# Kernel optimization log

Measured on AMD Instinct MI355X. Metric: run time of the kernel, lower is better.

The kernel has to match this reference:

```python
import jax, jax.numpy as jnp
import numpy as np

N_WAY = 5
K_SHOT = 5
TEMPERATURE = 2.0
EPS = 1e-8


def _l2norm(x, axis):
    n = jnp.sqrt(jnp.sum(x * x, axis=axis, keepdims=True))
    return x / jnp.maximum(n, EPS)


def setup_inputs() -> dict:
    key = jax.random.key(0)
    k1, k2, k3, k4 = jax.random.split(key, 4)
    b, q, c, h, w = 4, 75, 640, 14, 14
    s = N_WAY * K_SHOT
    return {
        "support_xf": jax.random.normal(k1, (b, s, c, h, w), dtype=jnp.float32),
        "support_y": jax.random.randint(k2, (b, s), 0, N_WAY),
        "query_xf": jax.random.normal(k3, (b, q, c, h, w), dtype=jnp.float32),
        "query_y": jax.random.randint(k4, (b, q), 0, N_WAY),
    }


def _mn4_loss(support_xf, query_xf, query_y):
    b, q, c, h, w = query_xf.shape
    M = h * w  # M_q == M_s (k_shot averaging)
    # k-shot average: (b, N, k, c, h*w) -> (b, N, c, M)
    sup = support_xf.reshape(b, N_WAY, K_SHOT, c, M).mean(axis=2)
    qf = query_xf.reshape(b, q, c, M)
    # cosine similarity: normalize along channel dim
    sup_n = _l2norm(sup, axis=2)   # (b, N, c, M)
    qf_n = _l2norm(qf, axis=2)     # (b, q, c, M)
    # S: (b, q, N, M_q, M_s)
    S = jnp.einsum('bqcm,bncs->bqnms', qf_n, sup_n)

    NM = N_WAY * M
    # merged: (b, q, M_q, N*M_s)
    merged = jnp.transpose(S, (0, 1, 3, 2, 4)).reshape(b, q, M, NM)
    query_nearest = jnp.argmax(merged, axis=-1)               # (b, q, M_q)
    class_wise_max = S.max(axis=-1).max(axis=2) + 1.0          # (b, q, M_q)
    class_m = jax.nn.one_hot(query_nearest, NM, dtype=S.dtype) * class_wise_max[..., None]  # (b,q,M_q,NM)
    class_m_max = class_m.max(axis=-2)                         # (b, q, NM)
    support_nearest = jnp.argmax(class_m, axis=-2)             # (b, q, NM)
    support_nearest = jnp.where(class_m_max == 0, M + 1, support_nearest)
    # gather: back-pointer for each query position's chosen support index
    gathered = jnp.take_along_axis(support_nearest, query_nearest, axis=-1)  # (b, q, M_q)
    mask = (gathered == jnp.arange(M)[None, None, :])          # mutual-NN mask (b, q, M_q)
    query_mask = mask.astype(S.dtype) * TEMPERATURE

    # predict: masked sum of per-class best similarities over query positions
    predict = (S.max(axis=-1) * query_mask[:, :, None, :]).sum(axis=-1)  # (b, q, N)
    predict = predict.reshape(b * q, N_WAY)
    y = query_y.reshape(b * q)
    logp = jax.nn.log_softmax(predict, axis=-1)
    loss = -jnp.take_along_axis(logp, y[:, None], axis=1).mean()
    return loss


def reference(support_xf, support_y, query_xf, query_y):
    return _mn4_loss(support_xf, query_xf, query_y)
```

## Files before the change

kernel.cpp:

```cpp
#include <hip/hip_runtime.h>
#include <math.h>

#define NWAY 5
#define KSHOT 5
#define BB 4
#define QQ 75
#define CC 640
#define MM 196
#define BQ (BB*QQ)
#define MP 208
#define NCOL 1024
#define NREAL 980

#define BPK_OFF   0
#define BPK_SZF   (BB*NCOL*CC/2)
#define APK_OFF   (BPK_OFF + BPK_SZF)
#define APK_SZF   ((BQ*MP + 64)*CC/2)
#define GSTAT_OFF (APK_OFF + APK_SZF)
#define GSTAT_N   (BQ*NWAY*MP)
#define NRMS_OFF  (GSTAT_OFF + 2*GSTAT_N)
#define NRMS_SZ   (BB*NWAY*MM)
#define NRMQ_OFF  (NRMS_OFF + NRMS_SZ)
#define NRMQ_SZ   (BQ*MM)

typedef __attribute__((ext_vector_type(8))) _Float16 half8;
typedef __attribute__((ext_vector_type(4))) float floatx4;

__global__ void k_prep(const float* __restrict__ sx, const float* __restrict__ qx,
                       _Float16* __restrict__ Apk, _Float16* __restrict__ Bpk,
                       float* __restrict__ nrmq, float* __restrict__ nrms) {
    __shared__ float T[64 * 197];
    int t = threadIdx.x;
    int blk = blockIdx.x;
    if (blk < 3000) {
        int bq = blk / 10, cc = blk % 10;
        int c0 = cc * 64;
        const float* Q = qx + (size_t)bq * CC * MM + (size_t)c0 * MM;
        for (int idx = t; idx < 64 * MM; idx += 256) {
            int ci = idx / MM, m = idx - ci * MM;
            T[ci * 197 + m] = Q[idx];
        }
        __syncthreads();
        _Float16* out = Apk + (size_t)bq * MP * CC;
        int mloc = t >> 3, cj8 = t & 7;
        #pragma unroll
        for (int r = 0; r < 7; r++) {
            int mm = r * 32 + mloc;
            if (mm < MP) {
                half8 v;
                #pragma unroll
                for (int k = 0; k < 8; k++) {
                    float f = (mm < MM) ? T[(cj8 * 8 + k) * 197 + mm] : 0.f;
                    v[k] = (_Float16)f;
                }
                *(half8*)&out[(size_t)mm * CC + c0 + cj8 * 8] = v;
            }
        }
        if (t < MM) {
            float ss = 0.f;
            for (int ci = 0; ci < 64; ci++) { float v = T[ci * 197 + t]; ss += v * v; }
            atomicAdd(&nrmq[bq * MM + t], ss);
        }
    } else {
        int bb = blk - 3000;
        int bn = bb / 10, cc = bb % 10;
        int b = bn / NWAY, n = bn % NWAY;
        int c0 = cc * 64;
        const float* S = sx + (size_t)bn * KSHOT * CC * MM + (size_t)c0 * MM;
        for (int idx = t; idx < 64 * MM; idx += 256) {
            int ci = idx / MM, m = idx - ci * MM;
            float s = 0.f;
            #pragma unroll
            for (int k = 0; k < KSHOT; k++) s += S[(size_t)k * CC * MM + idx];
            T[ci * 197 + m] = s * 0.2f;
        }
        __syncthreads();
        _Float16* out = Bpk + ((size_t)b * NCOL + (size_t)n * MM) * CC;
        int mloc = t >> 3, cj8 = t & 7;
        #pragma unroll
        for (int r = 0; r < 7; r++) {
            int mm = r * 32 + mloc;
            if (mm < MM) {
                half8 v;
                #pragma unroll
                for (int k = 0; k < 8; k++)
                    v[k] = (_Float16)T[(cj8 * 8 + k) * 197 + mm];
                *(half8*)&out[(size_t)mm * CC + c0 + cj8 * 8] = v;
            }
        }
        if (t < MM) {
            float ss = 0.f;
            for (int ci = 0; ci < 64; ci++) { float v = T[ci * 197 + t]; ss += v * v; }
            atomicAdd(&nrms[bn * MM + t], ss);
        }
    }
}

__global__ __launch_bounds__(256, 3) void k_sim(
    const _Float16* __restrict__ Apk, const _Float16* __restrict__ Bpk,
    const float* __restrict__ nrms, unsigned long long* __restrict__ gstat)
{
    __shared__ __align__(16) _Float16 Lds[16384];
    int id = blockIdx.x;
    int x = id & 7, s = id >> 3;
    int sub = s & 15, bqg = s >> 4;
    int bq = x + (bqg << 3);
    if (bq >= BQ) return;
    int mblk = sub >> 3, cblk = sub & 7;
    int b = bq / QQ;

    int t = threadIdx.x, lane = t & 63, w = t >> 6;
    int q = lane >> 4, l15 = lane & 15;

    const _Float16* Ab = Apk + (size_t)bq * MP * CC + (size_t)(mblk * 128) * CC;
    const _Float16* Bb = Bpk + ((size_t)b * NCOL + (size_t)(cblk * 128)) * CC;
    const _Float16* base = (w < 2) ? Ab : Bb;

    int voff[8];
    #pragma unroll
    for (int p = 0; p < 8; p++) {
        int chunk = (w * 8 + p) * 64 + lane;
        if (chunk < 1024) {
            int m = chunk >> 3, j = chunk & 7;
            voff[p] = m * CC + ((j ^ (m & 7)) << 3);
        } else {
            int cb = chunk - 1024;
            int jl = cb >> 3, j = cb & 7;
            voff[p] = jl * CC + ((j ^ (jl & 7)) << 3);
        }
    }

    int arow[2], asw[2], brow[8], bsw[8];
    #pragma unroll
    for (int i = 0; i < 2; i++) {
        int m = w * 32 + i * 16 + l15;
        arow[i] = m * 64; asw[i] = m & 7;
    }
    #pragma unroll
    for (int jt = 0; jt < 8; jt++) {
        int jl = jt * 16 + l15;
        brow[jt] = 8192 + jl * 64; bsw[jt] = jl & 7;
    }

    floatx4 acc[2][8];
    #pragma unroll
    for (int i = 0; i < 2; i++)
        #pragma unroll
        for (int j = 0; j < 8; j++) acc[i][j] = (floatx4){0.f, 0.f, 0.f, 0.f};

    for (int c0 = 0; c0 < CC; c0 += 64) {
        #pragma unroll
        for (int p = 0; p < 8; p++)
            __builtin_amdgcn_global_load_lds(
                (const __attribute__((address_space(1))) void*)(base + voff[p] + c0),
                (__attribute__((address_space(3))) void*)(Lds + (w * 8 + p) * 512),
                16, 0, 0);
        __syncthreads();
        #pragma unroll
        for (int ks = 0; ks < 2; ks++) {
            int cj = ks * 4 + q;
            half8 af[2], bf[8];
            #pragma unroll
            for (int i = 0; i < 2; i++)
                af[i] = *(const half8*)&Lds[arow[i] + ((cj ^ asw[i]) << 3)];
            #pragma unroll
            for (int jt = 0; jt < 8; jt++)
                bf[jt] = *(const half8*)&Lds[brow[jt] + ((cj ^ bsw[jt]) << 3)];
            #pragma unroll
            for (int i = 0; i < 2; i++)
                #pragma unroll
                for (int jt = 0; jt < 8; jt++)
                    acc[i][jt] = __builtin_amdgcn_mfma_f32_16x16x32_f16(af[i], bf[jt], acc[i][jt], 0, 0, 0);
        }
        __syncthreads();
    }

    int wbase = cblk * 128;
    int clsLo = wbase / 196;
    float invv[8]; int ms8[8], isLo[8], valid[8];
    #pragma unroll
    for (int jt = 0; jt < 8; jt++) {
        int c = wbase + jt * 16 + l15;
        int cls = c / 196;
        ms8[jt] = c - cls * 196;
        isLo[jt] = (cls == clsLo);
        valid[jt] = (c < NREAL);
        invv[jt] = valid[jt] ? (1.0f / fmaxf(sqrtf(nrms[b * NREAL + c]), 1e-8f)) : 0.f;
    }
    #pragma unroll
    for (int i = 0; i < 2; i++) {
        #pragma unroll
        for (int r = 0; r < 4; r++) {
            unsigned long long keyLo = 0ULL, keyHi = 0ULL;
            #pragma unroll
            for (int jt = 0; jt < 8; jt++) {
                float v = acc[i][jt][r] * invv[jt];
                unsigned int ub = __float_as_uint(v);
                unsigned int su = (ub & 0x80000000u) ? ~ub : (ub | 0x80000000u);
                unsigned long long key = valid[jt]
                    ? (((unsigned long long)su << 32) |
                       (unsigned long long)(0xFFFFFFFFu - (unsigned int)ms8[jt]))
                    : 0ULL;
                if (isLo[jt]) keyLo = (key > keyLo) ? key : keyLo;
                else          keyHi = (key > keyHi) ? key : keyHi;
            }
            #pragma unroll
            for (int sft = 1; sft < 16; sft <<= 1) {
                unsigned long long oL = __shfl_xor(keyLo, sft, 64);
                unsigned long long oH = __shfl_xor(keyHi, sft, 64);
                if (oL > keyLo) keyLo = oL;
                if (oH > keyHi) keyHi = oH;
            }
            if (l15 == 0) {
                int gm = mblk * 128 + w * 32 + i * 16 + q * 4 + r;
                if (gm < MM) {
                    if (keyLo)
                        atomicMax(&gstat[((size_t)bq * NWAY + clsLo) * MP + gm], keyLo);
                    int clsHi = clsLo + 1;
                    if (keyHi && clsHi < NWAY)
                        atomicMax(&gstat[((size_t)bq * NWAY + clsHi) * MP + gm], keyHi);
                }
            }
        }
    }
}

__global__ void k_post(const unsigned long long* __restrict__ gstat,
                       const float* __restrict__ nrmq,
                       float* __restrict__ out, const int* __restrict__ qy) {
    int bq = blockIdx.x;
    int t = threadIdx.x;
    __shared__ float invq_s[MM];
    __shared__ float cm[NWAY * MM];
    __shared__ int   ca[NWAY * MM];
    __shared__ float gmax[MM];
    __shared__ int   jst[MM];
    __shared__ int   msk[MM];
    __shared__ float pred[NWAY];

    if (t < MM) invq_s[t] = 1.0f / fmaxf(sqrtf(nrmq[bq * MM + t]), 1e-8f);
    __syncthreads();

    for (int i = t; i < NWAY * MM; i += 256) {
        int n = i / MM, m = i - n * MM;
        unsigned long long key = gstat[((size_t)bq * NWAY + n) * MP + m];
        unsigned int hi = (unsigned int)(key >> 32);
        unsigned int bits = (hi & 0x80000000u) ? (hi ^ 0x80000000u) : ~hi;
        cm[i] = __uint_as_float(bits) * invq_s[m];
        ca[i] = (int)(0xFFFFFFFFu - (unsigned int)(key & 0xFFFFFFFFu));
    }
    __syncthreads();

    if (t < MM) {
        float bv = cm[t];
        int bj = ca[t];
        for (int n = 1; n < NWAY; n++) {
            float v = cm[n * MM + t];
            if (v > bv) { bv = v; bj = n * MM + ca[n * MM + t]; }
        }
        gmax[t] = bv; jst[t] = bj;
    }
    __syncthreads();

    if (t < MM) {
        int myj = jst[t];
        float myv = gmax[t];
        int lose = 0;
        for (int m2 = 0; m2 < MM; m2++) {
            if (jst[m2] == myj &&
                (gmax[m2] > myv || (gmax[m2] == myv && m2 < t))) lose = 1;
        }
        msk[t] = !lose;
    }
    __syncthreads();

    if (t < NWAY) {
        float p = 0.f;
        for (int m = 0; m < MM; m++) if (msk[m]) p += cm[t * MM + m];
        pred[t] = 2.0f * p;
    }
    __syncthreads();

    if (t == 0) {
        float pm = pred[0];
        for (int n = 1; n < NWAY; n++) pm = fmaxf(pm, pred[n]);
        float s = 0.f;
        for (int n = 0; n < NWAY; n++) s += expf(pred[n] - pm);
        float lse = pm + logf(s);
        int y = qy[bq];
        atomicAdd(out, (lse - pred[y]) * (1.0f / (BB * QQ)));
    }
}

extern "C" void kernel_launch(void* const* d_in, const int* in_sizes, int n_in,
                              void* d_out, int out_size, void* d_ws, size_t ws_size,
                              hipStream_t stream) {
    const float* sx = (const float*)d_in[0];
    const float* qx = (const float*)d_in[2];
    const int*   qy = (const int*)d_in[3];
    float* out = (float*)d_out;
    float* ws  = (float*)d_ws;

    _Float16* Bpk = (_Float16*)(ws + BPK_OFF);
    _Float16* Apk = (_Float16*)(ws + APK_OFF);
    unsigned long long* gstat = (unsigned long long*)(ws + GSTAT_OFF);
    float* nrms = ws + NRMS_OFF;
    float* nrmq = ws + NRMQ_OFF;

    hipMemsetAsync(gstat, 0, (size_t)(2 * GSTAT_N + NRMS_SZ + NRMQ_SZ) * 4, stream);
    hipMemsetAsync(out, 0, 4, stream);
    hipLaunchKernelGGL(k_prep, dim3(3200), dim3(256), 0, stream, sx, qx, Apk, Bpk, nrmq, nrms);
    hipLaunchKernelGGL(k_sim,  dim3(8 * 38 * 16), dim3(256), 0, stream, Apk, Bpk, nrms, gstat);
    hipLaunchKernelGGL(k_post, dim3(300), dim3(256), 0, stream, gstat, nrmq, out, qy);
}
```

Baseline: 447.0 us.

## Retile k_sim GEMM to 256x256 blocks with double-buffered LDS loads

Restructures the similarity GEMM so that each 512-thread block computes all 256 (padded) query rows against 256 support columns, replacing the earlier 128x128 tiles. The new tiling cuts redundant A/B reloads from global memory. LDS is double-buffered so the next 64-channel slice is prefetched while MFMAs run on the current one. The change also remaps block order per XCD, skips MFMA tiles for padded query rows, raises wave priority around the MFMAs, and only reduces the second-class key when a wave's column range crosses a class boundary. In exchange, LDS use rises to 128KB per block and each thread holds a larger accumulator set, which limits occupancy and may cause spills.

Result: slower. 1.070 ms (+139.4%).

```diff
diff --git a/kernel.cpp b/kernel.cpp
--- a/kernel.cpp
+++ b/kernel.cpp
@@ -96,128 +96,144 @@
     }
 }
 
-__global__ __launch_bounds__(256, 3) void k_sim(
+__global__ __launch_bounds__(512, 2) void k_sim(
     const _Float16* __restrict__ Apk, const _Float16* __restrict__ Bpk,
     const float* __restrict__ nrms, unsigned long long* __restrict__ gstat)
 {
-    __shared__ __align__(16) _Float16 Lds[16384];
-    int id = blockIdx.x;
-    int x = id & 7, s = id >> 3;
-    int sub = s & 15, bqg = s >> 4;
-    int bq = x + (bqg << 3);
-    if (bq >= BQ) return;
-    int mblk = sub >> 3, cblk = sub & 7;
+    __shared__ __align__(16) _Float16 Lds[65536];
+
+    int hw = blockIdx.x;
+    int logical = (hw & 7) * 150 + (hw >> 3);
+    int bq = logical >> 2, cblk = logical & 3;
     int b = bq / QQ;
 
-    int t = threadIdx.x, lane = t & 63, w = t >> 6;
-    int q = lane >> 4, l15 = lane & 15;
-
-    const _Float16* Ab = Apk + (size_t)bq * MP * CC + (size_t)(mblk * 128) * CC;
-    const _Float16* Bb = Bpk + ((size_t)b * NCOL + (size_t)(cblk * 128)) * CC;
-    const _Float16* base = (w < 2) ? Ab : Bb;
-
-    int voff[8];
+    int t = threadIdx.x, w = t >> 6, lane = t & 63;
+    int wm = w >> 2, wn = w & 3;
+    int q = lane >> 4, l15 = lane & 15, s7 = l15 & 7;
+
+    const _Float16* Ab = Apk + (size_t)bq * MP * CC;
+    const _Float16* Bb = Bpk + ((size_t)b * NCOL + (size_t)cblk * 256) * CC;
+
+    int voff[4];
+    {
+        int rr = t >> 3, slot = t & 7;
+        #pragma unroll
+        for (int a = 0; a < 4; a++) {
+            int r = a * 64 + rr;
+            voff[a] = r * CC + ((slot ^ (r & 7)) << 3);
+        }
+    }
+
+    int aoff[8], boff[4];
     #pragma unroll
-    for (int p = 0; p < 8; p++) {
-        int chunk = (w * 8 + p) * 64 + lane;
-        if (chunk < 1024) {
-            int m = chunk >> 3, j = chunk & 7;
-            voff[p] = m * CC + ((j ^ (m & 7)) << 3);
-        } else {
-            int cb = chunk - 1024;
-            int jl = cb >> 3, j = cb & 7;
-            voff[p] = jl * CC + ((j ^ (jl & 7)) << 3);
-        }
-    }
-
-    int arow[2], asw[2], brow[8], bsw[8];
+    for (int m = 0; m < 8; m++) aoff[m] = (wm * 128 + m * 16 + l15) * 64;
     #pragma unroll
-    for (int i = 0; i < 2; i++) {
-        int m = w * 32 + i * 16 + l15;
-        arow[i] = m * 64; asw[i] = m & 7;
-    }
+    for (int n = 0; n < 4; n++) boff[n] = 16384 + (wn * 64 + n * 16 + l15) * 64;
+
+    floatx4 acc[8][4];
     #pragma unroll
-    for (int jt = 0; jt < 8; jt++) {
-        int jl = jt * 16 + l15;
-        brow[jt] = 8192 + jl * 64; bsw[jt] = jl & 7;
-    }
-
-    floatx4 acc[2][8];
+    for (int m = 0; m < 8; m++)
+        #pragma unroll
+        for (int n = 0; n < 4; n++) acc[m][n] = (floatx4){0.f, 0.f, 0.f, 0.f};
+
+    #define STAGE(TT)                                                                  \
+        do {                                                                           \
+            int nb_ = ((TT) & 1) << 15;                                                \
+            int c0_ = (TT) * 64;                                                       \
+            _Pragma("unroll")                                                          \
+            for (int a = 0; a < 4; a++) {                                              \
+                __builtin_amdgcn_global_load_lds(                                      \
+                    (const __attribute__((address_space(1))) void*)(Ab + voff[a] + c0_),\
+                    (__attribute__((address_space(3))) void*)(Lds + nb_ + a * 4096 + w * 512), \
+                    16, 0, 0);                                                         \
+                __builtin_amdgcn_global_load_lds(                                      \
+                    (const __attribute__((address_space(1))) void*)(Bb + voff[a] + c0_),\
+                    (__attribute__((address_space(3))) void*)(Lds + nb_ + 16384 + a * 4096 + w * 512), \
+                    16, 0, 0);                                                         \
+            }                                                                          \
+        } while (0)
+
+    STAGE(0);
+    __syncthreads();
+
+    for (int tt = 0; tt < 10; tt++) {
+        int cb = (tt & 1) << 15;
+        if (tt < 9) STAGE(tt + 1);
+
+        half8 bf[4][2];
+        #pragma unroll
+        for (int n = 0; n < 4; n++)
+            #pragma unroll
+            for (int ks = 0; ks < 2; ks++)
+                bf[n][ks] = *(const half8*)&Lds[cb + boff[n] + (((ks * 4 + q) ^ s7) << 3)];
+
+        __builtin_amdgcn_s_setprio(1);
+        #define MFMA_BLOCK(MTOP)                                                       \
+            _Pragma("unroll")                                                          \
+            for (int m = 0; m < (MTOP); m++) {                                         \
+                half8 af0 = *(const half8*)&Lds[cb + aoff[m] + ((q ^ s7) << 3)];       \
+                half8 af1 = *(const half8*)&Lds[cb + aoff[m] + (((4 + q) ^ s7) << 3)]; \
+                _Pragma("unroll")                                                      \
+                for (int n = 0; n < 4; n++) {                                          \
+                    acc[m][n] = __builtin_amdgcn_mfma_f32_16x16x32_f16(af0, bf[n][0], acc[m][n], 0, 0, 0); \
+                    acc[m][n] = __builtin_amdgcn_mfma_f32_16x16x32_f16(af1, bf[n][1], acc[m][n], 0, 0, 0); \
+                }                                                                      \
+            }
+        if (wm == 0) { MFMA_BLOCK(8) } else { MFMA_BLOCK(5) }
+        __builtin_amdgcn_s_setprio(0);
+
+        __syncthreads();
+    }
+
+    int wbase = cblk * 256 + wn * 64;
+    int clsLo = wbase / 196;
+    int clsHi = clsLo + 1;
+    bool hasHi = (((wbase + 63) / 196) != clsLo) && (clsHi < NWAY);
+    float invv[4]; int msv[4], isLo[4], valid[4];
     #pragma unroll
-    for (int i = 0; i < 2; i++)
-        #pragma unroll
-        for (int j = 0; j < 8; j++) acc[i][j] = (floatx4){0.f, 0.f, 0.f, 0.f};
-
-    for (int c0 = 0; c0 < CC; c0 += 64) {
-        #pragma unroll
-        for (int p = 0; p < 8; p++)
-            __builtin_amdgcn_global_load_lds(
-                (const __attribute__((address_space(1))) void*)(base + voff[p] + c0),
-                (__attribute__((address_space(3))) void*)(Lds + (w * 8 + p) * 512),
-                16, 0, 0);
-        __syncthreads();
-        #pragma unroll
-        for (int ks = 0; ks < 2; ks++) {
-            int cj = ks * 4 + q;
-            half8 af[2], bf[8];
-            #pragma unroll
-            for (int i = 0; i < 2; i++)
-                af[i] = *(const half8*)&Lds[arow[i] + ((cj ^ asw[i]) << 3)];
-            #pragma unroll
-            for (int jt = 0; jt < 8; jt++)
-                bf[jt] = *(const half8*)&Lds[brow[jt] + ((cj ^ bsw[jt]) << 3)];
-            #pragma unroll
-            for (int i = 0; i < 2; i++)
-                #pragma unroll
-                for (int jt = 0; jt < 8; jt++)
-                    acc[i][jt] = __builtin_amdgcn_mfma_f32_16x16x32_f16(af[i], bf[jt], acc[i][jt], 0, 0, 0);
-        }
-        __syncthreads();
-    }
-
-    int wbase = cblk * 128;
-    int clsLo = wbase / 196;
-    float invv[8]; int ms8[8], isLo[8], valid[8];
-    #pragma unroll
-    for (int jt = 0; jt < 8; jt++) {
-        int c = wbase + jt * 16 + l15;
+    for (int n = 0; n < 4; n++) {
+        int c = wbase + n * 16 + l15;
         int cls = c / 196;
-        ms8[jt] = c - cls * 196;
-        isLo[jt] = (cls == clsLo);
-        valid[jt] = (c < NREAL);
-        invv[jt] = valid[jt] ? (1.0f / fmaxf(sqrtf(nrms[b * NREAL + c]), 1e-8f)) : 0.f;
-    }
-    #pragma unroll
-    for (int i = 0; i < 2; i++) {
+        msv[n] = c - cls * 196;
+        isLo[n] = (cls == clsLo);
+        valid[n] = (c < NREAL);
+        invv[n] = valid[n] ? (1.0f / fmaxf(sqrtf(nrms[b * NREAL + c]), 1e-8f)) : 0.f;
+    }
+    int mtop = (wm == 0) ? 8 : 5;
+    for (int m = 0; m < mtop; m++) {
         #pragma unroll
         for (int r = 0; r < 4; r++) {
             unsigned long long keyLo = 0ULL, keyHi = 0ULL;
             #pragma unroll
-            for (int jt = 0; jt < 8; jt++) {
-                float v = acc[i][jt][r] * invv[jt];
+            for (int n = 0; n < 4; n++) {
+                float v = acc[m][n][r] * invv[n];
                 unsigned int ub = __float_as_uint(v);
                 unsigned int su = (ub & 0x80000000u) ? ~ub : (ub | 0x80000000u);
-                unsigned long long key = valid[jt]
+                unsigned long long key = valid[n]
                     ? (((unsigned long long)su << 32) |
-                       (unsigned long long)(0xFFFFFFFFu - (unsigned int)ms8[jt]))
+                       (unsigned long long)(0xFFFFFFFFu - (unsigned int)msv[n]))
                     : 0ULL;
-                if (isLo[jt]) keyLo = (key > keyLo) ? key : keyLo;
-                else          keyHi = (key > keyHi) ? key : keyHi;
+                if (isLo[n]) keyLo = (key > keyLo) ? key : keyLo;
+                else         keyHi = (key > keyHi) ? key : keyHi;
             }
             #pragma unroll
             for (int sft = 1; sft < 16; sft <<= 1) {
-                unsigned long long oL = __shfl_xor(keyLo, sft, 64);
-                unsigned long long oH = __shfl_xor(keyHi, sft, 64);
-                if (oL > keyLo) keyLo = oL;
-                if (oH > keyHi) keyHi = oH;
+                unsigned long long o = __shfl_xor(keyLo, sft, 64);
+                if (o > keyLo) keyLo = o;
+            }
+            if (hasHi) {
+                #pragma unroll
+                for (int sft = 1; sft < 16; sft <<= 1) {
+                    unsigned long long o = __shfl_xor(keyHi, sft, 64);
+                    if (o > keyHi) keyHi = o;
+                }
             }
             if (l15 == 0) {
-                int gm = mblk * 128 + w * 32 + i * 16 + q * 4 + r;
+                int gm = wm * 128 + m * 16 + q * 4 + r;
                 if (gm < MM) {
                     if (keyLo)
                         atomicMax(&gstat[((size_t)bq * NWAY + clsLo) * MP + gm], keyLo);
-                    int clsHi = clsLo + 1;
-                    if (keyHi && clsHi < NWAY)
+                    if (hasHi && keyHi)
                         atomicMax(&gstat[((size_t)bq * NWAY + clsHi) * MP + gm], keyHi);
                 }
             }
@@ -310,6 +326,6 @@
     hipMemsetAsync(gstat, 0, (size_t)(2 * GSTAT_N + NRMS_SZ + NRMQ_SZ) * 4, stream);
     hipMemsetAsync(out, 0, 4, stream);
     hipLaunchKernelGGL(k_prep, dim3(3200), dim3(256), 0, stream, sx, qx, Apk, Bpk, nrmq, nrms);
-    hipLaunchKernelGGL(k_sim,  dim3(8 * 38 * 16), dim3(256), 0, stream, Apk, Bpk, nrms, gstat);
+    hipLaunchKernelGGL(k_sim,  dim3(1200), dim3(512), 0, stream, Apk, Bpk, nrms, gstat);
     hipLaunchKernelGGL(k_post, dim3(300), dim3(256), 0, stream, gstat, nrmq, out, qy);
 }
```

## Cover all query rows per block, load A directly, double-buffer B tiles

Applied to the files above, without the earlier changes.

The similarity GEMM block now covers all 208 query rows instead of 128. It halves the grid and drops the mblk split, so each B column tile is loaded once per query. A fragments are read straight from global memory into registers, and only the B tile goes through LDS with double buffering, so the next chunk's async load overlaps the MFMAs. Waves take interleaved 16-row strips, rotated by cblk, so that only one wave does the fourth strip. The cost is more accumulators (4x8 floatx4), launch bounds lowered to 2 blocks per CU, and uncoalesced-ish direct global reads for A.

New measurement: 463.5 us. 3.7% more time.

```diff
diff --git a/kernel.cpp b/kernel.cpp
--- a/kernel.cpp
+++ b/kernel.cpp
@@ -96,81 +96,91 @@
     }
 }
 
-__global__ __launch_bounds__(256, 3) void k_sim(
+__global__ __launch_bounds__(256, 2) void k_sim(
     const _Float16* __restrict__ Apk, const _Float16* __restrict__ Bpk,
     const float* __restrict__ nrms, unsigned long long* __restrict__ gstat)
 {
     __shared__ __align__(16) _Float16 Lds[16384];
     int id = blockIdx.x;
     int x = id & 7, s = id >> 3;
-    int sub = s & 15, bqg = s >> 4;
+    int cblk = s & 7, bqg = s >> 3;
     int bq = x + (bqg << 3);
     if (bq >= BQ) return;
-    int mblk = sub >> 3, cblk = sub & 7;
     int b = bq / QQ;
 
     int t = threadIdx.x, lane = t & 63, w = t >> 6;
-    int q = lane >> 4, l15 = lane & 15;
-
-    const _Float16* Ab = Apk + (size_t)bq * MP * CC + (size_t)(mblk * 128) * CC;
+    int q = lane >> 4, l15 = lane & 15, s7 = l15 & 7;
+    int ws = (w + cblk) & 3;
+    const bool full = (ws == 0);
+
+    const _Float16* Ab = Apk + (size_t)bq * MP * CC;
     const _Float16* Bb = Bpk + ((size_t)b * NCOL + (size_t)(cblk * 128)) * CC;
-    const _Float16* base = (w < 2) ? Ab : Bb;
-
-    int voff[8];
-    #pragma unroll
-    for (int p = 0; p < 8; p++) {
-        int chunk = (w * 8 + p) * 64 + lane;
-        if (chunk < 1024) {
-            int m = chunk >> 3, j = chunk & 7;
-            voff[p] = m * CC + ((j ^ (m & 7)) << 3);
-        } else {
-            int cb = chunk - 1024;
-            int jl = cb >> 3, j = cb & 7;
-            voff[p] = jl * CC + ((j ^ (jl & 7)) << 3);
-        }
-    }
-
-    int arow[2], asw[2], brow[8], bsw[8];
-    #pragma unroll
-    for (int i = 0; i < 2; i++) {
-        int m = w * 32 + i * 16 + l15;
-        arow[i] = m * 64; asw[i] = m & 7;
-    }
-    #pragma unroll
-    for (int jt = 0; jt < 8; jt++) {
-        int jl = jt * 16 + l15;
-        brow[jt] = 8192 + jl * 64; bsw[jt] = jl & 7;
-    }
-
-    floatx4 acc[2][8];
-    #pragma unroll
-    for (int i = 0; i < 2; i++)
+
+    const _Float16* arow[4];
+    #pragma unroll
+    for (int i = 0; i < 4; i++)
+        arow[i] = Ab + (size_t)((ws + 4 * i) * 16 + l15) * CC + q * 8;
+
+    int voffb[4];
+    #pragma unroll
+    for (int p = 0; p < 4; p++) {
+        int jl = (p * 256 + t) >> 3, j = t & 7;
+        voffb[p] = jl * CC + ((j ^ (jl & 7)) << 3);
+    }
+
+    int brow[8];
+    #pragma unroll
+    for (int jt = 0; jt < 8; jt++)
+        brow[jt] = (jt * 16 + l15) * 64;
+
+    floatx4 acc[4][8];
+    #pragma unroll
+    for (int i = 0; i < 4; i++)
         #pragma unroll
         for (int j = 0; j < 8; j++) acc[i][j] = (floatx4){0.f, 0.f, 0.f, 0.f};
 
-    for (int c0 = 0; c0 < CC; c0 += 64) {
-        #pragma unroll
-        for (int p = 0; p < 8; p++)
-            __builtin_amdgcn_global_load_lds(
-                (const __attribute__((address_space(1))) void*)(base + voff[p] + c0),
-                (__attribute__((address_space(3))) void*)(Lds + (w * 8 + p) * 512),
-                16, 0, 0);
-        __syncthreads();
+    #pragma unroll
+    for (int p = 0; p < 4; p++)
+        __builtin_amdgcn_global_load_lds(
+            (const __attribute__((address_space(1))) void*)(Bb + voffb[p]),
+            (__attribute__((address_space(3))) void*)(Lds + p * 2048 + w * 512),
+            16, 0, 0);
+    __syncthreads();
+
+    for (int tt = 0; tt < 10; tt++) {
+        int cb = (tt & 1) << 13;
+
+        half8 af[4][2];
+        #pragma unroll
+        for (int i = 0; i < 4; i++) {
+            if (i == 3 && !full) continue;
+            #pragma unroll
+            for (int ks = 0; ks < 2; ks++)
+                af[i][ks] = *(const half8*)(arow[i] + tt * 64 + ks * 32);
+        }
+
+        if (tt < 9) {
+            int nb = ((tt + 1) & 1) << 13;
+            #pragma unroll
+            for (int p = 0; p < 4; p++)
+                __builtin_amdgcn_global_load_lds(
+                    (const __attribute__((address_space(1))) void*)(Bb + voffb[p] + (tt + 1) * 64),
+                    (__attribute__((address_space(3))) void*)(Lds + nb + p * 2048 + w * 512),
+                    16, 0, 0);
+        }
+
         #pragma unroll
         for (int ks = 0; ks < 2; ks++) {
             int cj = ks * 4 + q;
-            half8 af[2], bf[8];
-            #pragma unroll
-            for (int i = 0; i < 2; i++)
-                af[i] = *(const half8*)&Lds[arow[i] + ((cj ^ asw[i]) << 3)];
-            #pragma unroll
-            for (int jt = 0; jt < 8; jt++)
-                bf[jt] = *(const half8*)&Lds[brow[jt] + ((cj ^ bsw[jt]) << 3)];
-            #pragma unroll
-            for (int i = 0; i < 2; i++)
+            #pragma unroll
+            for (int jt = 0; jt < 8; jt++) {
+                half8 bf = *(const half8*)&Lds[cb + brow[jt] + ((cj ^ s7) << 3)];
                 #pragma unroll
-                for (int jt = 0; jt < 8; jt++)
-                    acc[i][jt] = __builtin_amdgcn_mfma_f32_16x16x32_f16(af[i], bf[jt], acc[i][jt], 0, 0, 0);
+                for (int i = 0; i < 4; i++) {
+                    if (i == 3 && !full) continue;
+                    acc[i][jt] = __builtin_amdgcn_mfma_f32_16x16x32_f16(af[i][ks], bf, acc[i][jt], 0, 0, 0);
+                }
+            }
         }
         __syncthreads();
     }
@@ -188,7 +198,8 @@
         invv[jt] = valid[jt] ? (1.0f / fmaxf(sqrtf(nrms[b * NREAL + c]), 1e-8f)) : 0.f;
     }
     #pragma unroll
-    for (int i = 0; i < 2; i++) {
+    for (int i = 0; i < 4; i++) {
+        if (i == 3 && !full) continue;
         #pragma unroll
         for (int r = 0; r < 4; r++) {
             unsigned long long keyLo = 0ULL, keyHi = 0ULL;
@@ -212,7 +223,7 @@
                 if (oH > keyHi) keyHi = oH;
             }
             if (l15 == 0) {
-                int gm = mblk * 128 + w * 32 + i * 16 + q * 4 + r;
+                int gm = (ws + 4 * i) * 16 + q * 4 + r;
                 if (gm < MM) {
                     if (keyLo)
                         atomicMax(&gstat[((size_t)bq * NWAY + clsLo) * MP + gm], keyLo);
@@ -310,6 +321,6 @@
     hipMemsetAsync(gstat, 0, (size_t)(2 * GSTAT_N + NRMS_SZ + NRMQ_SZ) * 4, stream);
     hipMemsetAsync(out, 0, 4, stream);
     hipLaunchKernelGGL(k_prep, dim3(3200), dim3(256), 0, stream, sx, qx, Apk, Bpk, nrmq, nrms);
-    hipLaunchKernelGGL(k_sim,  dim3(8 * 38 * 16), dim3(256), 0, stream, Apk, Bpk, nrms, gstat);
+    hipLaunchKernelGGL(k_sim,  dim3(8 * 38 * 8), dim3(256), 0, stream, Apk, Bpk, nrms, gstat);
     hipLaunchKernelGGL(k_post, dim3(300), dim3(256), 0, stream, gstat, nrmq, out, qy);
 }
```
